# Kernel tuning notes

Measured on AMD Instinct MI355X. Metric: run time of the kernel, lower is better.

## Reference

```python
import jax, jax.numpy as jnp
from jax import lax
import numpy as np

V, EMB, ELMO, WORD, H, B, R, L = 11322, 300, 1024, 512, 512, 32, 10, 20


def setup_inputs():
    key = jax.random.key(0)
    ks = jax.random.split(key, 24)

    def n(k, shape, s=0.02):
        return jax.random.normal(k, shape, dtype=jnp.float32) * s

    inp = {}
    inp["ques"] = jax.random.randint(ks[0], (B, R, L), 0, V)
    inp["hist"] = jax.random.randint(ks[1], (B, R, 2 * L), 0, V)
    inp["ques_len"] = jax.random.randint(ks[2], (B, R), 1, L + 1)
    inp["hist_len"] = jax.random.randint(ks[3], (B, R), 1, 2 * L + 1)
    inp["img_feat"] = n(ks[4], (B, 36, 2048), 1.0)
    inp["v_relations"] = n(ks[5], (B, 36, 36, 512), 1.0)
    inp["w_emb"] = n(ks[6], (V, EMB))          # GloVe/numberbatch table
    inp["elmo_emb"] = n(ks[7], (V, ELMO))      # frozen ELMo table
    inp["Wc"] = n(ks[8], (WORD, ELMO))         # embed_change Linear
    inp["bc"] = jnp.zeros((WORD,), jnp.float32)
    IN0 = EMB + WORD                            # LSTM layer-0 input size = 812
    names = ["q_Wih0", "q_Whh0", "q_b0", "q_Wih1", "q_Whh1", "q_b1",
             "h_Wih0", "h_Whh0", "h_b0", "h_Wih1", "h_Whh1", "h_b1"]
    shapes = [(4 * H, IN0), (4 * H, H), (4 * H,), (4 * H, H), (4 * H, H), (4 * H,)] * 2
    for i, (nm, sh) in enumerate(zip(names, shapes)):
        inp[nm] = n(ks[9 + i], sh, 0.04)
    return inp


def lstm_layer(x, Wih, Whh, b):
    # x: [N, T, In] -> all hidden states [N, T, H]; PyTorch gate order i,f,g,o
    N = x.shape[0]
    Hh = Whh.shape[1]
    xproj = jnp.einsum('nti,gi->ntg', x, Wih) + b  # [N, T, 4H]

    def step(carry, xp):
        h, c = carry
        gates = xp + h @ Whh.T
        i, f, g, o = jnp.split(gates, 4, axis=-1)
        c = jax.nn.sigmoid(f) * c + jax.nn.sigmoid(i) * jnp.tanh(g)
        h = jax.nn.sigmoid(o) * jnp.tanh(c)
        return (h, c), h

    h0 = jnp.zeros((N, Hh), x.dtype)
    _, hs = lax.scan(step, (h0, h0), jnp.swapaxes(xproj, 0, 1))
    return jnp.swapaxes(hs, 0, 1)


def encode(tokens, lens, w_emb, elmo_emb, Wc, bc, Wih0, Whh0, b0, Wih1, Whh1, b1):
    # Embedding lookup + elmo->word projection, 2-layer LSTM, take h at t = len-1
    Ntok = tokens.shape[0]
    emb = w_emb[tokens]                         # [N, T, 300]
    elmo = elmo_emb[tokens] @ Wc.T + bc         # [N, T, 512] (dropout off: eval)
    x = jnp.concatenate([emb, elmo], axis=-1)   # [N, T, 812]
    h1 = lstm_layer(x, Wih0, Whh0, b0)
    h2 = lstm_layer(h1, Wih1, Whh1, b1)
    return h2[jnp.arange(Ntok), lens - 1]       # DynamicRNN: last valid hidden


def reference(ques, hist, ques_len, hist_len, img_feat, v_relations, w_emb, elmo_emb, Wc, bc,
              q_Wih0, q_Whh0, q_b0, q_Wih1, q_Whh1, q_b1,
              h_Wih0, h_Whh0, h_b0, h_Wih1, h_Whh1, h_b1):
    Bq, Rr, Ll = ques.shape
    ques_embed = encode(ques.reshape(Bq * Rr, Ll), ques_len.reshape(-1),
                        w_emb, elmo_emb, Wc, bc,
                        q_Wih0, q_Whh0, q_b0, q_Wih1, q_Whh1, q_b1).reshape(Bq, Rr, -1)
    hist_embed = encode(hist.reshape(Bq * Rr, 2 * Ll), hist_len.reshape(-1),
                        w_emb, elmo_emb, Wc, bc,
                        h_Wih0, h_Whh0, h_b0, h_Wih1, h_Whh1, h_b1).reshape(Bq, Rr, -1)
    # Vectorized form of the Python double loop + pad_sequence:
    # f_history[b, i, j] = hist_embed[b, j] if j <= i else 0   -> [B, R, R, H]
    tri = jnp.tril(jnp.ones((Rr, Rr), hist_embed.dtype))
    f_history = hist_embed[:, None, :, :] * tri[None, :, :, None]
    # masks exactly as t_rel.abs().sum(-1).bool() on the broadcast tensors
    m = (jnp.abs(f_history).sum(-1) != 0)       # [B, R, R]
    # t_rel[b,i,j,k,:] = f_history[b,i,j,:] zeroed where tmp (=f_history[b,i,k]) is zero
    t_rel = f_history[:, :, :, None, :] * m[:, :, None, :, None]
    tmp = f_history[:, :, None, :, :] * m[:, :, :, None, None]
    text_rel = jnp.concatenate([t_rel, tmp], axis=-1)  # [B, R, R, R, 2H]
    return ques_embed, text_rel
```

## Files before the change

### kernel.cpp

```cpp
#include <hip/hip_runtime.h>
#include <math.h>

#define NSEQ 320
#define HDIM 512
#define G4   2048
#define EMBD 300
#define ELMOD 1024
#define XPAD 832
#define BUFU (160*1024)

typedef __attribute__((ext_vector_type(8))) short bf16x8;
typedef __attribute__((ext_vector_type(4))) float f32x4;
typedef __attribute__((ext_vector_type(4))) unsigned int u32x4;
typedef __attribute__((ext_vector_type(2))) unsigned int u32x2;
typedef unsigned short ushort_t;

__device__ __forceinline__ float sigmoidf_(float x) { return 1.0f / (1.0f + expf(-x)); }

__device__ __forceinline__ ushort_t f2bf(float f) {
    unsigned u = __float_as_uint(f);
    u = (u + 0x7FFFu + ((u >> 16) & 1u)) >> 16;
    return (ushort_t)u;
}
__device__ __forceinline__ unsigned pack2(float a, float b) {
    return (unsigned)f2bf(a) | ((unsigned)f2bf(b) << 16);
}

struct ConvPack {
    const float* src[9];
    ushort_t* dst[9];
    int srcCols[9], dstStride[9], dstOff[9], fillCols[9];
    long base[10];
};

__global__ __launch_bounds__(256) void conv_all_kernel(ConvPack P)
{
    long gid = (long)blockIdx.x * 256 + threadIdx.x;
    if (gid >= P.base[9]) return;
    int job = 0;
    #pragma unroll
    for (int j = 1; j < 9; ++j) if (gid >= P.base[j]) job = j;
    int e  = (int)(gid - P.base[job]);
    int fc = P.fillCols[job];
    int r  = e / fc;
    int ci = e - r * fc;
    int sc = P.srcCols[job];
    float v = (ci < sc) ? P.src[job][(size_t)r * sc + ci] : 0.0f;
    P.dst[job][(size_t)r * P.dstStride[job] + P.dstOff[job] + ci] = f2bf(v);
}

__global__ __launch_bounds__(128) void emb_gather_kernel(
    const int* __restrict__ ques, const int* __restrict__ hist,
    const float* __restrict__ w_emb, ushort_t* __restrict__ Xb)
{
    int n = blockIdx.x;
    int tokid = (n < 6400) ? ques[n] : hist[n - 6400];
    int t = threadIdx.x;
    ushort_t* dst = Xb + (size_t)n * XPAD;
    if (t < 75) {
        const float4* src = (const float4*)(w_emb + (size_t)tokid * EMBD);
        float4 v = src[t];
        dst[4*t+0] = f2bf(v.x); dst[4*t+1] = f2bf(v.y);
        dst[4*t+2] = f2bf(v.z); dst[4*t+3] = f2bf(v.w);
    } else if (t >= 108) {
        dst[812 + (t - 108)] = 0;
    }
}

__global__ __launch_bounds__(256) void gemm_ff_kernel(
    const ushort_t* __restrict__ Ab, const float* __restrict__ Af,
    const int* __restrict__ tok, int strideA,
    const ushort_t* __restrict__ W, const float* __restrict__ bias,
    ushort_t* __restrict__ C, int strideC, int K, int remap)
{
    __shared__ ushort_t As[64 * 40];
    __shared__ ushort_t Bs[64 * 40];
    const int m0 = blockIdx.y * 64;
    const int n0 = blockIdx.x * 64;
    const int tid = threadIdx.x;
    const int r  = tid >> 2;
    const int kq = (tid & 3) << 3;

    const ushort_t* arow_b = nullptr;
    const float*    arow_f = nullptr;
    if (Af) arow_f = Af + (size_t)tok[m0 + r] * strideA + kq;
    else    arow_b = Ab + (size_t)(m0 + r) * strideA + kq;
    const ushort_t* brow = W + (size_t)(n0 + r) * K + kq;

    const int lane = tid & 63;
    const int w = tid >> 6;
    const int wm = w & 1, wn = w >> 1;
    const int kc = (lane >> 4) << 3;

    f32x4 acc[2][2];
    #pragma unroll
    for (int f = 0; f < 2; ++f)
        #pragma unroll
        for (int g = 0; g < 2; ++g)
            acc[f][g] = (f32x4){0.f, 0.f, 0.f, 0.f};

    for (int k0 = 0; k0 < K; k0 += 32) {
        if (Af) {
            float4 v0 = ((const float4*)(arow_f + k0))[0];
            float4 v1 = ((const float4*)(arow_f + k0))[1];
            uint4 p; p.x = pack2(v0.x, v0.y); p.y = pack2(v0.z, v0.w);
            p.z = pack2(v1.x, v1.y); p.w = pack2(v1.z, v1.w);
            *(uint4*)&As[r*40 + kq] = p;
        } else {
            *(uint4*)&As[r*40 + kq] = *(const uint4*)(arow_b + k0);
        }
        *(uint4*)&Bs[r*40 + kq] = *(const uint4*)(brow + k0);
        __syncthreads();
        bf16x8 af[2], bfr[2];
        #pragma unroll
        for (int f = 0; f < 2; ++f)
            af[f] = *(const bf16x8*)&As[(wm*32 + f*16 + (lane & 15))*40 + kc];
        #pragma unroll
        for (int g = 0; g < 2; ++g)
            bfr[g] = *(const bf16x8*)&Bs[(wn*32 + g*16 + (lane & 15))*40 + kc];
        #pragma unroll
        for (int f = 0; f < 2; ++f)
            #pragma unroll
            for (int g = 0; g < 2; ++g)
                acc[f][g] = __builtin_amdgcn_mfma_f32_16x16x32_bf16(af[f], bfr[g], acc[f][g], 0, 0, 0);
        __syncthreads();
    }

    #pragma unroll
    for (int f = 0; f < 2; ++f) {
        #pragma unroll
        for (int g = 0; g < 2; ++g) {
            int col = n0 + wn*32 + g*16 + (lane & 15);
            float bv = bias[col];
            int colw = remap ? ((col & 511) * 4 + (col >> 9)) : col;
            #pragma unroll
            for (int i = 0; i < 4; ++i) {
                int row = m0 + wm*32 + f*16 + ((lane >> 4) << 2) + i;
                C[(size_t)row * strideC + colw] = f2bf(acc[f][g][i] + bv);
            }
        }
    }
}

struct PCellN {
    ushort_t* rot;
    const ushort_t* B;
    const ushort_t* xp;
    const float* bias;
    float* hlast;
    const int* lens;
    int* flags;
    int* pflag;
    int K, T, layer;
};
struct PPackN { PCellN cell[8]; };

template<int N> __device__ __forceinline__ void vmwait() {
    if constexpr      (N == 0)  asm volatile("s_waitcnt vmcnt(0)"  ::: "memory");
    else if constexpr (N == 1)  asm volatile("s_waitcnt vmcnt(1)"  ::: "memory");
    else if constexpr (N == 2)  asm volatile("s_waitcnt vmcnt(2)"  ::: "memory");
    else if constexpr (N == 3)  asm volatile("s_waitcnt vmcnt(3)"  ::: "memory");
    else if constexpr (N == 4)  asm volatile("s_waitcnt vmcnt(4)"  ::: "memory");
    else if constexpr (N == 5)  asm volatile("s_waitcnt vmcnt(5)"  ::: "memory");
    else if constexpr (N == 6)  asm volatile("s_waitcnt vmcnt(6)"  ::: "memory");
    else if constexpr (N == 7)  asm volatile("s_waitcnt vmcnt(7)"  ::: "memory");
    else if constexpr (N == 8)  asm volatile("s_waitcnt vmcnt(8)"  ::: "memory");
    else if constexpr (N == 9)  asm volatile("s_waitcnt vmcnt(9)"  ::: "memory");
    else if constexpr (N == 10) asm volatile("s_waitcnt vmcnt(10)" ::: "memory");
    else if constexpr (N == 11) asm volatile("s_waitcnt vmcnt(11)" ::: "memory");
    else if constexpr (N == 12) asm volatile("s_waitcnt vmcnt(12)" ::: "memory");
    else if constexpr (N == 13) asm volatile("s_waitcnt vmcnt(13)" ::: "memory");
    else if constexpr (N == 14) asm volatile("s_waitcnt vmcnt(14)" ::: "memory");
    else                        asm volatile("s_waitcnt vmcnt(15)" ::: "memory");
}

template<int C, int NQ, int D>
__device__ __forceinline__ void aissN(uint4 (&ap)[D][NQ],
    const ushort_t* baseX, const ushort_t* baseH, const int* aoff)
{
    const ushort_t* b_ = (C * 32 < 512) ? baseX : baseH;
    #pragma unroll
    for (int q = 0; q < NQ; ++q)
        asm volatile("global_load_dwordx4 %0, %1, off"
            : "=v"(ap[C % D][q])
            : "v"((const char*)b_ + aoff[q] + C * 64));
}

template<int C, int D, int NQ>
__device__ __forceinline__ void prologueN(uint4 (&ap)[D][NQ],
    const ushort_t* bX, const ushort_t* bH, const int* aoff)
{
    if constexpr (C < D) {
        aissN<C, NQ, D>(ap, bX, bH, aoff);
        prologueN<C + 1, D, NQ>(ap, bX, bH, aoff);
    }
}

template<int C, int NC, int NQ, int D>
__device__ __forceinline__ void chunksN(uint4 (&ap)[D][NQ], f32x4 (&acc)[NQ][4],
    const ushort_t* bX, const ushort_t* bH, const int* aoff,
    const ushort_t* Bs, int cc, int kg, int swz)
{
    if constexpr (C < NC) {
        constexpr int infl = (NC - 1 - C) > (D - 1) ? (D - 1) : (NC - 1 - C);
        vmwait<infl * NQ>();
        __builtin_amdgcn_sched_barrier(0);
        bf16x8 bfr[4];
        #pragma unroll
        for (int g = 0; g < 4; ++g) {
            int boff = ((g*16 + cc) * (NC*64) + C*64 + kg*16) ^ swz;
            bfr[g] = *(const bf16x8*)((const char*)Bs + boff);
        }
        #pragma unroll
        for (int q = 0; q < NQ; ++q)
            #pragma unroll
            for (int g = 0; g < 4; ++g)
                acc[q][g] = __builtin_amdgcn_mfma_f32_16x16x32_bf16(
                    *(const bf16x8*)&ap[C % D][q], bfr[g], acc[q][g], 0, 0, 0);
        if constexpr (C + D < NC) aissN<C + D, NQ, D>(ap, bX, bH, aoff);
        chunksN<C + 1, NC, NQ, D>(ap, acc, bX, bH, aoff, Bs, cc, kg, swz);
    }
}

template<int NC, int NQ, int D>
__device__ __forceinline__ void step_work(
    const ushort_t* __restrict__ baseX,
    const ushort_t* __restrict__ baseH,
    const ushort_t* __restrict__ Bs,
    const ushort_t* __restrict__ xp,
    const float* __restrict__ bias_r,
    ushort_t* __restrict__ Ost,
    float* __restrict__ hlast,
    const unsigned* __restrict__ lr,
    float (&creg)[3][4],
    int t, int T, int tq0, int lane, int j)
{
    const int cc = lane & 15, kg = lane >> 4;
    const int swz = (cc & 7) << 4;

    int aoff[NQ];
    #pragma unroll
    for (int q = 0; q < NQ; ++q)
        aoff[q] = ((tq0 + q)*16 + cc)*2048 + kg*16;

    u32x2 xpk[NQ][4];
    if (xp) {
        #pragma unroll
        for (int q = 0; q < NQ; ++q)
            #pragma unroll
            for (int i = 0; i < 4; ++i) {
                const int n = (tq0 + q)*16 + kg*4 + i;
                asm volatile("global_load_dwordx2 %0, %1, off"
                    : "=v"(xpk[q][i])
                    : "v"((const char*)xp + ((size_t)n*T + t)*4096 + (size_t)j*8));
            }
    }

    f32x4 acc[NQ][4];
    #pragma unroll
    for (int q = 0; q < NQ; ++q)
        #pragma unroll
        for (int g = 0; g < 4; ++g)
            acc[q][g] = (f32x4){0.f, 0.f, 0.f, 0.f};

    uint4 ap[D][NQ];
    prologueN<0, D, NQ>(ap, baseX, baseH, aoff);
    chunksN<0, NC, NQ, D>(ap, acc, baseX, baseH, aoff, Bs, cc, kg, swz);
    __builtin_amdgcn_sched_barrier(0);

    #pragma unroll
    for (int q = 0; q < NQ; ++q) {
        const unsigned lq = lr[q];
        #pragma unroll
        for (int i = 0; i < 4; ++i) {
            const int n = (tq0 + q)*16 + kg*4 + i;
            float g0 = acc[q][0][i], g1 = acc[q][1][i];
            float g2 = acc[q][2][i], g3 = acc[q][3][i];
            if (xp) {
                u32x2 xv = xpk[q][i];
                g0 += __uint_as_float(xv.x << 16);
                g1 += __uint_as_float(xv.x & 0xFFFF0000u);
                g2 += __uint_as_float(xv.y << 16);
                g3 += __uint_as_float(xv.y & 0xFFFF0000u);
            } else {
                g0 += bias_r[0]; g1 += bias_r[1];
                g2 += bias_r[2]; g3 += bias_r[3];
            }
            float cn = sigmoidf_(g1) * creg[q][i] + sigmoidf_(g0) * tanhf(g2);
            creg[q][i] = cn;
            float h = sigmoidf_(g3) * tanhf(cn);
            unsigned hb = (unsigned)f2bf(h);
            unsigned pb = (unsigned)__shfl_xor((int)hb, 1);
            if ((cc & 1) == 0) {
                ushort_t* oa = Ost + (size_t)n * 1024 + j;
                asm volatile("global_store_dword %0, %1, off sc0 sc1"
                             :: "v"(oa), "v"(hb | (pb << 16)));
            }
            if (hlast && t == (int)((lq >> (8*i)) & 0xFF) - 1)
                hlast[(size_t)n * HDIM + j] = h;
        }
    }
}

__global__ __launch_bounds__(256) void lstm_persist_kernel(PPackN P)
{
    const int inst = blockIdx.x & 7;
    const int blk  = blockIdx.x >> 3;
    const PCellN cl = P.cell[inst];

    const int tid  = threadIdx.x;
    const int w    = tid >> 6;
    const int lane = tid & 63;
    const int cc   = lane & 15;
    const int kg   = lane >> 4;
    const int j0   = blk * 16;
    const int j    = j0 + cc;
    const int K = cl.K, T = cl.T;
    const int nq  = (w < 2) ? 3 : 2;
    const int tq0 = (w < 2) ? w*3 : 6 + (w - 2)*2;

    __shared__ ushort_t Bs[64 * 1024];

    {
        const int CH = K >> 3;
        const int tot = 64 * CH;
        for (int idx = tid; idx < tot; idx += 256) {
            int r = idx / CH, ch = idx - r * CH;
            int gr = (r >> 4) * HDIM + j0 + (r & 15);
            int dst = (idx * 16) ^ ((r & 7) << 4);
            *(u32x4*)((char*)Bs + dst) = *(const u32x4*)(cl.B + (size_t)gr * K + ch * 8);
        }
    }

    float bias_r[4] = {0.f, 0.f, 0.f, 0.f};
    if (cl.bias) {
        #pragma unroll
        for (int g = 0; g < 4; ++g) bias_r[g] = cl.bias[g * HDIM + j];
    }

    unsigned lr[3] = {0u, 0u, 0u};
    #pragma unroll
    for (int q = 0; q < 3; ++q) {
        if (q < nq) {
            unsigned pkd = 0;
            #pragma unroll
            for (int i = 0; i < 4; ++i)
                pkd |= ((unsigned)cl.lens[(tq0 + q)*16 + kg*4 + i] & 0xFF) << (8*i);
            lr[q] = pkd;
        }
    }

    float creg[3][4];
    #pragma unroll
    for (int q = 0; q < 3; ++q)
        #pragma unroll
        for (int i = 0; i < 4; ++i) creg[q][i] = 0.f;

    __syncthreads();

    for (int ss = 0; ss <= T; ++ss) {
        const bool active = cl.layer ? (ss >= 1) : (ss < T);
        if (active) {
            const int t = cl.layer ? (ss - 1) : ss;
            const ushort_t* baseX; const ushort_t* baseH; ushort_t* Ost;
            if (cl.layer == 0) {
                baseX = cl.rot + (size_t)t * BUFU;
                baseH = baseX;
                Ost   = cl.rot + (size_t)(t + 1) * BUFU;
            } else {
                baseX = cl.rot + (size_t)(t + 1) * BUFU;
                baseH = cl.rot + (size_t)t * BUFU;
                Ost   = cl.rot + (size_t)(t + 1) * BUFU + HDIM;
            }
            if (K == 512) {
                if (w < 2) step_work<16,3,6>(baseX, baseH, Bs, cl.xp, bias_r, Ost, cl.hlast, lr, creg, t, T, tq0, lane, j);
                else       step_work<16,2,8>(baseX, baseH, Bs, cl.xp, bias_r, Ost, cl.hlast, lr, creg, t, T, tq0, lane, j);
            } else {
                if (w < 2) step_work<32,3,6>(baseX, baseH, Bs, cl.xp, bias_r, Ost, cl.hlast, lr, creg, t, T, tq0, lane, j);
                else       step_work<32,2,8>(baseX, baseH, Bs, cl.xp, bias_r, Ost, cl.hlast, lr, creg, t, T, tq0, lane, j);
            }
        }
        if (ss < T) {
            asm volatile("s_waitcnt vmcnt(0)" ::: "memory");
            __syncthreads();
            if (tid == 0) {
                int* fa = cl.flags + blk;
                int vv = ss + 1;
                asm volatile("global_store_dword %0, %1, off sc0 sc1"
                             :: "v"(fa), "v"(vv) : "memory");
            }
            if (w == 0) {
                const int* fa = cl.flags + (lane & 31);
                int spins = 0; bool ok;
                do {
                    int v;
                    asm volatile("global_load_dword %0, %1, off sc0 sc1"
                                 : "=v"(v) : "v"(fa) : "memory");
                    asm volatile("s_waitcnt vmcnt(0)" ::: "memory");
                    ok = (bool)__all(v >= ss + 1);
                    if (!ok) __builtin_amdgcn_s_sleep(1);
                } while (!ok && ++spins < (1 << 20));
                if (cl.layer == 0) {
                    if (blk == 0 && lane == 0) {
                        int vv = ss + 1;
                        asm volatile("global_store_dword %0, %1, off sc0 sc1"
                                     :: "v"(cl.pflag), "v"(vv) : "memory");
                    }
                } else if (lane == 0) {
                    int spins2 = 0; int pv;
                    do {
                        asm volatile("global_load_dword %0, %1, off sc0 sc1"
                                     : "=v"(pv) : "v"((const int*)cl.pflag) : "memory");
                        asm volatile("s_waitcnt vmcnt(0)" ::: "memory");
                        if (pv < ss + 1) __builtin_amdgcn_s_sleep(1);
                    } while (pv < ss + 1 && ++spins2 < (1 << 20));
                }
            }
            __syncthreads();
        }
    }
}

__global__ __launch_bounds__(64) void nz_kernel(
    const float* __restrict__ he, int* __restrict__ nz)
{
    int rr = blockIdx.x;
    int lane = threadIdx.x;
    const float* row = he + (size_t)rr * HDIM;
    bool any = false;
    for (int k = lane; k < HDIM; k += 64) any |= (row[k] != 0.0f);
    unsigned long long b = __ballot(any);
    if (lane == 0) nz[rr] = (b != 0ull) ? 1 : 0;
}

__global__ __launch_bounds__(256) void expand_kernel(
    const float* __restrict__ he, const int* __restrict__ nz,
    float* __restrict__ out)
{
    int blk = blockIdx.x;
    int k = blk % 10;
    int j = (blk / 10) % 10;
    int i = (blk / 100) % 10;
    int b = blk / 1000;
    int tid = threadIdx.x;
    float4* o = (float4*)(out + (size_t)blk * 1024);
    float4 z; z.x = z.y = z.z = z.w = 0.0f;
    if (tid < 128) {
        bool m = (j <= i) && (k <= i) && (nz[b*10 + k] != 0);
        float4 v = m ? ((const float4*)(he + (size_t)(b*10 + j) * HDIM))[tid] : z;
        o[tid] = v;
    } else {
        int c = tid - 128;
        bool m = (k <= i) && (j <= i) && (nz[b*10 + j] != 0);
        float4 v = m ? ((const float4*)(he + (size_t)(b*10 + k) * HDIM))[c] : z;
        o[128 + c] = v;
    }
}

extern "C" void kernel_launch(void* const* d_in, const int* in_sizes, int n_in,
                              void* d_out, int out_size, void* d_ws, size_t ws_size,
                              hipStream_t stream)
{
    (void)in_sizes; (void)n_in; (void)out_size; (void)ws_size;
    const int* ques     = (const int*)d_in[0];
    const int* hist     = (const int*)d_in[1];
    const int* ques_len = (const int*)d_in[2];
    const int* hist_len = (const int*)d_in[3];
    const float* w_emb  = (const float*)d_in[6];
    const float* elmo   = (const float*)d_in[7];
    const float* Wc     = (const float*)d_in[8];
    const float* bc     = (const float*)d_in[9];

    char* ws = (char*)d_ws;
    size_t off = 0;
    auto alloc = [&](size_t bytes) { char* p = ws + off; off += (bytes + 255) & ~(size_t)255; return p; };
    ushort_t* XP0bf = (ushort_t*)alloc((size_t)19200 * G4 * 2);

    const size_t rotSlice = (size_t)41 * BUFU * 2;
    char* uni = alloc(4 * rotSlice);
    ushort_t* Xb = (ushort_t*)uni;
    auto rotPtr = [&](int s, int v) { return (ushort_t*)(uni + (size_t)(s*2 + v) * rotSlice); };

    ushort_t* Wcb = (ushort_t*)alloc((size_t)HDIM * ELMOD * 2);
    ushort_t *Wih0b[2], *Whh0b[2], *Wcat[2];
    for (int s = 0; s < 2; ++s) {
        Wih0b[s] = (ushort_t*)alloc((size_t)G4 * XPAD * 2);
        Whh0b[s] = (ushort_t*)alloc((size_t)G4 * HDIM * 2);
        Wcat[s]  = (ushort_t*)alloc((size_t)G4 * ELMOD * 2);
    }
    int* ctrs = (int*)alloc(4096);
    float* he = (float*)alloc((size_t)NSEQ * HDIM * 4);
    int* nzb  = (int*)alloc(NSEQ * 4);

    float* out = (float*)d_out;
    float* ques_embed = out;
    float* text_rel   = out + (size_t)NSEQ * HDIM;

    const int rowoff[2] = {0, 6400};
    const int TT[2] = {20, 40};
    const int* lensp[2] = {ques_len, hist_len};

    ConvPack CP;
    {
        int ji = 0; long base = 0;
        auto addJob = [&](const float* src, ushort_t* dst, int sc, int ds, int doff, int fc, int rows) {
            CP.src[ji] = src; CP.dst[ji] = dst; CP.srcCols[ji] = sc; CP.dstStride[ji] = ds;
            CP.dstOff[ji] = doff; CP.fillCols[ji] = fc; CP.base[ji] = base;
            base += (long)fc * rows; ++ji;
        };
        addJob(Wc, Wcb, ELMOD, ELMOD, 0, ELMOD, HDIM);
        for (int s = 0; s < 2; ++s) {
            addJob((const float*)d_in[10 + 6*s], Wih0b[s], 812,  XPAD,  0,    XPAD, G4);
            addJob((const float*)d_in[11 + 6*s], Whh0b[s], HDIM, HDIM,  0,    HDIM, G4);
            addJob((const float*)d_in[13 + 6*s], Wcat[s],  HDIM, ELMOD, 0,    HDIM, G4);
            addJob((const float*)d_in[14 + 6*s], Wcat[s],  HDIM, ELMOD, HDIM, HDIM, G4);
        }
        CP.base[9] = base;
        int nblk = (int)((base + 255) / 256);
        conv_all_kernel<<<nblk, 256, 0, stream>>>(CP);
    }

    emb_gather_kernel<<<19200, 128, 0, stream>>>(ques, hist, w_emb, Xb);
    for (int s = 0; s < 2; ++s) {
        int Ntok = NSEQ * TT[s];
        ushort_t* XbS = Xb + (size_t)rowoff[s] * XPAD;
        const int* tok = s ? hist : ques;
        gemm_ff_kernel<<<dim3(HDIM/64, Ntok/64), 256, 0, stream>>>(
            nullptr, elmo, tok, ELMOD, Wcb, bc, XbS + EMBD, XPAD, ELMOD, 0);
        const float* b0 = (const float*)d_in[12 + 6*s];
        gemm_ff_kernel<<<dim3(G4/64, Ntok/64), 256, 0, stream>>>(
            XbS, nullptr, nullptr, XPAD, Wih0b[s], b0,
            XP0bf + (size_t)rowoff[s] * G4, G4, XPAD, 1);
    }

    hipMemsetAsync(ctrs, 0, 4096, stream);
    for (int s = 0; s < 2; ++s)
        for (int v = 0; v < 2; ++v)
            hipMemsetAsync(rotPtr(s, v), 0, (size_t)BUFU * 2, stream);

    PPackN P;
    for (int layer = 0; layer < 2; ++layer)
        for (int s = 0; s < 2; ++s)
            for (int v = 0; v < 2; ++v) {
                int inst = layer*4 + s*2 + v;
                PCellN& c = P.cell[inst];
                c.rot   = rotPtr(s, v);
                c.B     = layer ? Wcat[s] : Whh0b[s];
                c.xp    = layer ? nullptr
                                : XP0bf + (size_t)(rowoff[s] + v*160*TT[s]) * G4;
                c.bias  = layer ? (const float*)d_in[15 + 6*s] : nullptr;
                c.hlast = layer ? ((s ? he : ques_embed) + (size_t)v*160*HDIM) : nullptr;
                c.lens  = lensp[s] + v*160;
                c.flags = ctrs + inst * 32;
                c.pflag = ctrs + 512 + (s*2 + v) * 32;
                c.K = layer ? ELMOD : HDIM;
                c.T = TT[s];
                c.layer = layer;
            }
    lstm_persist_kernel<<<256, 256, 0, stream>>>(P);

    nz_kernel<<<NSEQ, 64, 0, stream>>>(he, nzb);
    expand_kernel<<<32000, 256, 0, stream>>>(he, nzb, text_rel);
}
```

Before: 991.5 us.

## Split persistent LSTM columns to 8 per block and double block count

Each persistent LSTM block now owns 8 hidden columns instead of 16, so the grid grows from 256 to 512 blocks and two blocks can share a CU. The weight slice held in LDS is halved and stored with padded rows instead of an XOR swizzle. Each lane computes two gate pre-activations and swaps them with a neighbour lane to assemble all four LSTM gates. The per-step MFMA work per block shrinks, but the grid-wide flag barrier now has twice as many participants, which adds synchronisation cost.

```diff
diff --git a/kernel.cpp b/kernel.cpp
--- a/kernel.cpp
+++ b/kernel.cpp
@@ -197,28 +197,27 @@
 }
 
 template<int C, int NC, int NQ, int D>
-__device__ __forceinline__ void chunksN(uint4 (&ap)[D][NQ], f32x4 (&acc)[NQ][4],
+__device__ __forceinline__ void chunksN(uint4 (&ap)[D][NQ], f32x4 (&acc)[NQ][2],
     const ushort_t* bX, const ushort_t* bH, const int* aoff,
-    const ushort_t* Bs, int cc, int kg, int swz)
+    const ushort_t* Bs, int cc, int kg)
 {
     if constexpr (C < NC) {
+        constexpr int PK = NC * 32 + 16;
         constexpr int infl = (NC - 1 - C) > (D - 1) ? (D - 1) : (NC - 1 - C);
         vmwait<infl * NQ>();
         __builtin_amdgcn_sched_barrier(0);
-        bf16x8 bfr[4];
-        #pragma unroll
-        for (int g = 0; g < 4; ++g) {
-            int boff = ((g*16 + cc) * (NC*64) + C*64 + kg*16) ^ swz;
-            bfr[g] = *(const bf16x8*)((const char*)Bs + boff);
-        }
-        #pragma unroll
-        for (int q = 0; q < NQ; ++q)
-            #pragma unroll
-            for (int g = 0; g < 4; ++g)
-                acc[q][g] = __builtin_amdgcn_mfma_f32_16x16x32_bf16(
-                    *(const bf16x8*)&ap[C % D][q], bfr[g], acc[q][g], 0, 0, 0);
+        bf16x8 bfr[2];
+        bfr[0] = *(const bf16x8*)&Bs[cc * PK + C*32 + kg*8];
+        bfr[1] = *(const bf16x8*)&Bs[(16 + cc) * PK + C*32 + kg*8];
+        #pragma unroll
+        for (int q = 0; q < NQ; ++q) {
+            acc[q][0] = __builtin_amdgcn_mfma_f32_16x16x32_bf16(
+                *(const bf16x8*)&ap[C % D][q], bfr[0], acc[q][0], 0, 0, 0);
+            acc[q][1] = __builtin_amdgcn_mfma_f32_16x16x32_bf16(
+                *(const bf16x8*)&ap[C % D][q], bfr[1], acc[q][1], 0, 0, 0);
+        }
         if constexpr (C + D < NC) aissN<C + D, NQ, D>(ap, bX, bH, aoff);
-        chunksN<C + 1, NC, NQ, D>(ap, acc, bX, bH, aoff, Bs, cc, kg, swz);
+        chunksN<C + 1, NC, NQ, D>(ap, acc, bX, bH, aoff, Bs, cc, kg);
     }
 }
 
@@ -228,7 +227,7 @@
     const ushort_t* __restrict__ baseH,
     const ushort_t* __restrict__ Bs,
     const ushort_t* __restrict__ xp,
-    const float* __restrict__ bias_r,
+    float b0, float b1,
     ushort_t* __restrict__ Ost,
     float* __restrict__ hlast,
     const unsigned* __restrict__ lr,
@@ -236,7 +235,7 @@
     int t, int T, int tq0, int lane, int j)
 {
     const int cc = lane & 15, kg = lane >> 4;
-    const int swz = (cc & 7) << 4;
+    const int half = cc >> 3;
 
     int aoff[NQ];
     #pragma unroll
@@ -256,16 +255,16 @@
             }
     }
 
-    f32x4 acc[NQ][4];
-    #pragma unroll
-    for (int q = 0; q < NQ; ++q)
-        #pragma unroll
-        for (int g = 0; g < 4; ++g)
-            acc[q][g] = (f32x4){0.f, 0.f, 0.f, 0.f};
+    f32x4 acc[NQ][2];
+    #pragma unroll
+    for (int q = 0; q < NQ; ++q) {
+        acc[q][0] = (f32x4){0.f, 0.f, 0.f, 0.f};
+        acc[q][1] = (f32x4){0.f, 0.f, 0.f, 0.f};
+    }
 
     uint4 ap[D][NQ];
     prologueN<0, D, NQ>(ap, baseX, baseH, aoff);
-    chunksN<0, NC, NQ, D>(ap, acc, baseX, baseH, aoff, Bs, cc, kg, swz);
+    chunksN<0, NC, NQ, D>(ap, acc, baseX, baseH, aoff, Bs, cc, kg);
     __builtin_amdgcn_sched_barrier(0);
 
     #pragma unroll
@@ -274,35 +273,40 @@
         #pragma unroll
         for (int i = 0; i < 4; ++i) {
             const int n = (tq0 + q)*16 + kg*4 + i;
-            float g0 = acc[q][0][i], g1 = acc[q][1][i];
-            float g2 = acc[q][2][i], g3 = acc[q][3][i];
+            float v0 = acc[q][0][i];
+            float v1 = acc[q][1][i];
             if (xp) {
                 u32x2 xv = xpk[q][i];
-                g0 += __uint_as_float(xv.x << 16);
-                g1 += __uint_as_float(xv.x & 0xFFFF0000u);
-                g2 += __uint_as_float(xv.y << 16);
-                g3 += __uint_as_float(xv.y & 0xFFFF0000u);
+                v0 += half ? __uint_as_float(xv.x & 0xFFFF0000u)
+                           : __uint_as_float(xv.x << 16);
+                v1 += half ? __uint_as_float(xv.y & 0xFFFF0000u)
+                           : __uint_as_float(xv.y << 16);
             } else {
-                g0 += bias_r[0]; g1 += bias_r[1];
-                g2 += bias_r[2]; g3 += bias_r[3];
-            }
-            float cn = sigmoidf_(g1) * creg[q][i] + sigmoidf_(g0) * tanhf(g2);
+                v0 += b0; v1 += b1;
+            }
+            float p0 = __shfl_xor(v0, 8);
+            float p1 = __shfl_xor(v1, 8);
+            float gi = half ? p0 : v0;
+            float gf = half ? v0 : p0;
+            float gg = half ? p1 : v1;
+            float go = half ? v1 : p1;
+            float cn = sigmoidf_(gf) * creg[q][i] + sigmoidf_(gi) * tanhf(gg);
             creg[q][i] = cn;
-            float h = sigmoidf_(g3) * tanhf(cn);
+            float h = sigmoidf_(go) * tanhf(cn);
             unsigned hb = (unsigned)f2bf(h);
             unsigned pb = (unsigned)__shfl_xor((int)hb, 1);
-            if ((cc & 1) == 0) {
+            if (half == 0 && (cc & 1) == 0) {
                 ushort_t* oa = Ost + (size_t)n * 1024 + j;
                 asm volatile("global_store_dword %0, %1, off sc0 sc1"
                              :: "v"(oa), "v"(hb | (pb << 16)));
             }
-            if (hlast && t == (int)((lq >> (8*i)) & 0xFF) - 1)
+            if (hlast && half == 0 && t == (int)((lq >> (8*i)) & 0xFF) - 1)
                 hlast[(size_t)n * HDIM + j] = h;
         }
     }
 }
 
-__global__ __launch_bounds__(256) void lstm_persist_kernel(PPackN P)
+__global__ __launch_bounds__(256, 2) void lstm_persist_kernel(PPackN P)
 {
     const int inst = blockIdx.x & 7;
     const int blk  = blockIdx.x >> 3;
@@ -313,29 +317,29 @@
     const int lane = tid & 63;
     const int cc   = lane & 15;
     const int kg   = lane >> 4;
-    const int j0   = blk * 16;
-    const int j    = j0 + cc;
-    const int K = cl.K, T = cl.T;
+    const int half = cc >> 3;
+    const int j0   = blk * 8;
+    const int j    = j0 + (cc & 7);
+    const int K = cl.K, T = cl.T, PK = K + 16;
     const int nq  = (w < 2) ? 3 : 2;
     const int tq0 = (w < 2) ? w*3 : 6 + (w - 2)*2;
 
-    __shared__ ushort_t Bs[64 * 1024];
+    __shared__ ushort_t Bs[32 * 1040];
 
     {
         const int CH = K >> 3;
-        const int tot = 64 * CH;
+        const int tot = 32 * CH;
         for (int idx = tid; idx < tot; idx += 256) {
             int r = idx / CH, ch = idx - r * CH;
-            int gr = (r >> 4) * HDIM + j0 + (r & 15);
-            int dst = (idx * 16) ^ ((r & 7) << 4);
-            *(u32x4*)((char*)Bs + dst) = *(const u32x4*)(cl.B + (size_t)gr * K + ch * 8);
-        }
-    }
-
-    float bias_r[4] = {0.f, 0.f, 0.f, 0.f};
+            int gr = (r >> 3) * HDIM + j0 + (r & 7);
+            *(u32x4*)&Bs[r * PK + ch * 8] = *(const u32x4*)(cl.B + (size_t)gr * K + ch * 8);
+        }
+    }
+
+    float b0 = 0.f, b1 = 0.f;
     if (cl.bias) {
-        #pragma unroll
-        for (int g = 0; g < 4; ++g) bias_r[g] = cl.bias[g * HDIM + j];
+        b0 = cl.bias[half * HDIM + j];
+        b1 = cl.bias[(2 + half) * HDIM + j];
     }
 
     unsigned lr[3] = {0u, 0u, 0u};
@@ -373,11 +377,11 @@
                 Ost   = cl.rot + (size_t)(t + 1) * BUFU + HDIM;
             }
             if (K == 512) {
-                if (w < 2) step_work<16,3,6>(baseX, baseH, Bs, cl.xp, bias_r, Ost, cl.hlast, lr, creg, t, T, tq0, lane, j);
-                else       step_work<16,2,8>(baseX, baseH, Bs, cl.xp, bias_r, Ost, cl.hlast, lr, creg, t, T, tq0, lane, j);
+                if (w < 2) step_work<16,3,6>(baseX, baseH, Bs, cl.xp, b0, b1, Ost, cl.hlast, lr, creg, t, T, tq0, lane, j);
+                else       step_work<16,2,8>(baseX, baseH, Bs, cl.xp, b0, b1, Ost, cl.hlast, lr, creg, t, T, tq0, lane, j);
             } else {
-                if (w < 2) step_work<32,3,6>(baseX, baseH, Bs, cl.xp, bias_r, Ost, cl.hlast, lr, creg, t, T, tq0, lane, j);
-                else       step_work<32,2,8>(baseX, baseH, Bs, cl.xp, bias_r, Ost, cl.hlast, lr, creg, t, T, tq0, lane, j);
+                if (w < 2) step_work<32,3,6>(baseX, baseH, Bs, cl.xp, b0, b1, Ost, cl.hlast, lr, creg, t, T, tq0, lane, j);
+                else       step_work<32,2,8>(baseX, baseH, Bs, cl.xp, b0, b1, Ost, cl.hlast, lr, creg, t, T, tq0, lane, j);
             }
         }
         if (ss < T) {
@@ -390,7 +394,7 @@
                              :: "v"(fa), "v"(vv) : "memory");
             }
             if (w == 0) {
-                const int* fa = cl.flags + (lane & 31);
+                const int* fa = cl.flags + lane;
                 int spins = 0; bool ok;
                 do {
                     int v;
@@ -488,7 +492,7 @@
         Whh0b[s] = (ushort_t*)alloc((size_t)G4 * HDIM * 2);
         Wcat[s]  = (ushort_t*)alloc((size_t)G4 * ELMOD * 2);
     }
-    int* ctrs = (int*)alloc(4096);
+    int* ctrs = (int*)alloc(8192);
     float* he = (float*)alloc((size_t)NSEQ * HDIM * 4);
     int* nzb  = (int*)alloc(NSEQ * 4);
 
@@ -533,7 +537,7 @@
             XP0bf + (size_t)rowoff[s] * G4, G4, XPAD, 1);
     }
 
-    hipMemsetAsync(ctrs, 0, 4096, stream);
+    hipMemsetAsync(ctrs, 0, 8192, stream);
     for (int s = 0; s < 2; ++s)
         for (int v = 0; v < 2; ++v)
             hipMemsetAsync(rotPtr(s, v), 0, (size_t)BUFU * 2, stream);
@@ -551,13 +555,13 @@
                 c.bias  = layer ? (const float*)d_in[15 + 6*s] : nullptr;
                 c.hlast = layer ? ((s ? he : ques_embed) + (size_t)v*160*HDIM) : nullptr;
                 c.lens  = lensp[s] + v*160;
-                c.flags = ctrs + inst * 32;
-                c.pflag = ctrs + 512 + (s*2 + v) * 32;
+                c.flags = ctrs + inst * 64;
+                c.pflag = ctrs + 1024 + (s*2 + v) * 32;
                 c.K = layer ? ELMOD : HDIM;
                 c.T = TT[s];
                 c.layer = layer;
             }
-    lstm_persist_kernel<<<256, 256, 0, stream>>>(P);
+    lstm_persist_kernel<<<512, 256, 0, stream>>>(P);
 
     nz_kernel<<<NSEQ, 64, 0, stream>>>(he, nzb);
     expand_kernel<<<32000, 256, 0, stream>>>(he, nzb, text_rel);
```

New measurement: 1.451 ms. 46.3% more time.
